# Kernel tuning notes

Measured on AMD Instinct MI355X. Metric: run time of the kernel, lower is better.

## Reference

```python
import jax, jax.numpy as jnp
import numpy as np

WEIGHT = 1.0  # config['weight']


def setup_inputs() -> dict:
    key = jax.random.key(0)
    ks = jax.random.split(key, 10)
    B, N, S, C, D, E, H, V = 8, 4096, 512, 16, 1024, 256, 1024, 100000
    return {
        "span_vecs": jax.random.normal(ks[0], (B, N, D), jnp.float32),
        "ent_table": jax.random.normal(ks[1], (V, E), jnp.float32) * 0.02,
        "W1": jax.random.normal(ks[2], (D + E, H), jnp.float32) * (1.0 / np.sqrt(D + E)),
        "b1": jnp.zeros((H,), jnp.float32),
        "W2": jax.random.normal(ks[3], (H,), jnp.float32) * (1.0 / np.sqrt(H)),
        "b2": jnp.zeros((), jnp.float32),
        "targets_all": jax.random.uniform(ks[4], (B, N, C), jnp.float32),
        "linker_indices": jax.random.randint(ks[5], (B, S), 0, N, jnp.int32),
        "candidates_all": jax.random.randint(ks[6], (B, N, C), 0, V, jnp.int32),
        "candidate_lengths_all": jax.random.randint(ks[7], (B, N), 0, C + 1, jnp.int32),
    }


def reference(span_vecs, ent_table, W1, b1, W2, b2, targets_all,
              linker_indices, candidates_all, candidate_lengths_all):
    D = span_vecs.shape[-1]
    C = candidates_all.shape[-1]
    idx = linker_indices  # [B, S]

    # batched_index_select gathers over the span axis
    candidates = jnp.take_along_axis(candidates_all, idx[:, :, None], axis=1)        # [B,S,C] int
    lengths = jnp.take_along_axis(candidate_lengths_all, idx, axis=1)                # [B,S] int
    targets = jnp.take_along_axis(targets_all, idx[:, :, None], axis=1)              # [B,S,C]
    linker_vecs = jnp.take_along_axis(span_vecs, idx[:, :, None], axis=1)            # [B,S,D]

    cand_vecs = ent_table[candidates]                                                # [B,S,C,E]

    # layers: Linear(D+E,H) -> ReLU -> (dropout=identity in eval) -> Linear(H,1)
    # fused: split W1 so the [B,S,C,D+E] expanded concat is never materialized
    W1s, W1e = W1[:D], W1[D:]
    h_span = jnp.einsum('bsd,dh->bsh', linker_vecs, W1s)                             # [B,S,H]
    h_cand = jnp.einsum('bsce,eh->bsch', cand_vecs, W1e)                             # [B,S,C,H]
    h = jax.nn.relu(h_span[:, :, None, :] + h_cand + b1)
    scores = jnp.einsum('bsch,h->bsc', h, W2) + b2                                   # [B,S,C]

    # create_candidate_mask
    mask = (jnp.arange(C)[None, None, :] < lengths[:, :, None]).astype(scores.dtype)

    # BCEWithLogitsLoss(reduction='none'), masked sum * weight
    bce = jnp.maximum(scores, 0.0) - scores * targets + jnp.log1p(jnp.exp(-jnp.abs(scores)))
    loss = (mask * bce).sum() * WEIGHT

    predictions = jnp.argmax(scores - (1.0 - mask) * 1e23, axis=-1)                  # [B,S]
    return loss, scores, predictions
```

## Files before the change

kernel.cpp:

```cpp
#include <hip/hip_runtime.h>
#include <math.h>


typedef short short8 __attribute__((ext_vector_type(8)));
typedef float f32x16 __attribute__((ext_vector_type(16)));

static __device__ inline unsigned short f2bf(float x) {
  unsigned u = __float_as_uint(x);
  unsigned r = (u + 0x7FFFu + ((u >> 16) & 1u)) >> 16;
  return (unsigned short)r;
}
static __device__ inline float bf2f(unsigned short b) {
  return __uint_as_float(((unsigned)b) << 16);
}

#define GLD_TO_LDS(gp, lp)                                          \
  __builtin_amdgcn_global_load_lds(                                 \
      (const __attribute__((address_space(1))) void*)(gp),          \
      (__attribute__((address_space(3))) void*)(lp), 16, 0, 0)

__global__ __launch_bounds__(256) void k_prep2(const int* __restrict__ linker,
                                               const int* __restrict__ cand_all,
                                               int* __restrict__ cand_ids,
                                               int* __restrict__ span_rows) {
  int g = blockIdx.x * 256 + threadIdx.x;
  int pair = g >> 4;
  int b = pair >> 9;
  int i = linker[pair];
  cand_ids[g] = cand_all[(((size_t)b << 12) + (size_t)i) * 16 + (g & 15)];
  if (g < 4096) span_rows[g] = ((g >> 9) << 12) + linker[g];
}

template <int LOG4>
__global__ __launch_bounds__(256) void k_gsplit(const float* __restrict__ src,
                                                const int* __restrict__ rows,
                                                unsigned short* __restrict__ hi,
                                                unsigned short* __restrict__ lo) {
  int f = blockIdx.x * 256 + threadIdx.x;
  int row = f >> LOG4;
  int c4 = f & ((1 << LOG4) - 1);
  const float4 v =
      *((const float4*)(src + ((size_t)rows[row] << (LOG4 + 2))) + c4);
  unsigned short h0 = f2bf(v.x), h1 = f2bf(v.y), h2 = f2bf(v.z), h3 = f2bf(v.w);
  unsigned short l0 = f2bf(v.x - bf2f(h0)), l1 = f2bf(v.y - bf2f(h1));
  unsigned short l2 = f2bf(v.z - bf2f(h2)), l3 = f2bf(v.w - bf2f(h3));
  *(ushort4*)(hi + ((size_t)f << 2)) = make_ushort4(h0, h1, h2, h3);
  *(ushort4*)(lo + ((size_t)f << 2)) = make_ushort4(l0, l1, l2, l3);
}

__global__ __launch_bounds__(256) void k_w1t(const float* __restrict__ W1,
                                             unsigned short* __restrict__ sThi,
                                             unsigned short* __restrict__ sTlo,
                                             unsigned short* __restrict__ eThi,
                                             unsigned short* __restrict__ eTlo) {
  __shared__ float t[32][33];
  int n0 = blockIdx.x * 32, k0 = blockIdx.y * 32;
  int rr = threadIdx.x >> 5, cc = threadIdx.x & 31;
#pragma unroll
  for (int i = 0; i < 4; ++i)
    t[rr + 8 * i][cc] = W1[(size_t)(k0 + rr + 8 * i) * 1024 + n0 + cc];
  __syncthreads();
#pragma unroll
  for (int i = 0; i < 4; ++i) {
    int nl = rr + 8 * i;
    float v = t[cc][nl];
    unsigned short h = f2bf(v);
    unsigned short l = f2bf(v - bf2f(h));
    int n = n0 + nl, k = k0 + cc;
    if (k0 < 1024) {
      sThi[(size_t)n * 1024 + k] = h;
      sTlo[(size_t)n * 1024 + k] = l;
    } else {
      eThi[(size_t)n * 256 + (k - 1024)] = h;
      eTlo[(size_t)n * 256 + (k - 1024)] = l;
    }
  }
}

template <int KSTEPS, int RLA, int RLB, int MODE>
__global__ __launch_bounds__(256, 2) void k_g32(
    const unsigned short* __restrict__ Ahi, const unsigned short* __restrict__ Alo,
    const unsigned short* __restrict__ Bhi, const unsigned short* __restrict__ Blo,
    const float* __restrict__ HsIn, const float* __restrict__ b1,
    const float* __restrict__ W2, float* __restrict__ Out) {
  const int tid = threadIdx.x;
  const int l = tid & 63;
  const int w = tid >> 6;
  const int wm = w >> 1, wn = w & 1;
  const int id = blockIdx.x;
  const int m8 = id & 7;
  const int cb = (id >> 3) & 7;
  const int q = id >> 6;
  const int row0 = ((q << 3) + m8) << 7;
  const int col0 = cb << 7;

  __shared__ unsigned short lds[32768];

  f32x16 acc[2][2];
#pragma unroll
  for (int i = 0; i < 2; ++i)
#pragma unroll
    for (int j = 0; j < 2; ++j)
#pragma unroll
      for (int k = 0; k < 16; ++k) acc[i][j][k] = 0.f;

  const int ar0 = tid >> 2, ap0 = tid & 3;
  const int al0c = ap0 ^ ((ar0 >> 1) & 3);
  const int ar1 = (tid + 256) >> 2;
  const int al1c = ap0 ^ ((ar1 >> 1) & 3);
  const size_t aoff0 = (size_t)(row0 + ar0) * RLA + al0c * 8;
  const size_t aoff1 = (size_t)(row0 + ar1) * RLA + al1c * 8;
  const size_t boff0 = (size_t)(col0 + ar0) * RLB + al0c * 8;
  const size_t boff1 = (size_t)(col0 + ar1) * RLB + al1c * 8;
  const int w512 = w * 512;

  {
    unsigned short* b = lds;
    GLD_TO_LDS(Ahi + aoff0, b + w512);
    GLD_TO_LDS(Ahi + aoff1, b + 2048 + w512);
    GLD_TO_LDS(Alo + aoff0, b + 4096 + w512);
    GLD_TO_LDS(Alo + aoff1, b + 6144 + w512);
    GLD_TO_LDS(Bhi + boff0, b + 8192 + w512);
    GLD_TO_LDS(Bhi + boff1, b + 10240 + w512);
    GLD_TO_LDS(Blo + boff0, b + 12288 + w512);
    GLD_TO_LDS(Blo + boff1, b + 14336 + w512);
  }
  asm volatile("s_waitcnt vmcnt(0)" ::: "memory");
  __builtin_amdgcn_s_barrier();
  asm volatile("" ::: "memory");

  for (int ks = 0; ks < KSTEPS; ++ks) {
    if (ks + 1 < KSTEPS) {
      const int k0 = (ks + 1) * 32;
      unsigned short* b = lds + (((ks + 1) & 1) << 14);
      GLD_TO_LDS(Ahi + aoff0 + k0, b + w512);
      GLD_TO_LDS(Ahi + aoff1 + k0, b + 2048 + w512);
      GLD_TO_LDS(Alo + aoff0 + k0, b + 4096 + w512);
      GLD_TO_LDS(Alo + aoff1 + k0, b + 6144 + w512);
      GLD_TO_LDS(Bhi + boff0 + k0, b + 8192 + w512);
      GLD_TO_LDS(Bhi + boff1 + k0, b + 10240 + w512);
      GLD_TO_LDS(Blo + boff0 + k0, b + 12288 + w512);
      GLD_TO_LDS(Blo + boff1 + k0, b + 14336 + w512);
    }

    const unsigned short* cbuf = lds + ((ks & 1) << 14);
#pragma unroll
    for (int kc = 0; kc < 2; ++kc) {
      const int kg = kc * 2 + (l >> 5);
      short8 ah[2], alv[2], bh[2], bl[2];
#pragma unroll
      for (int it = 0; it < 2; ++it) {
        int r = wm * 64 + it * 32 + (l & 31);
        int off = r * 32 + ((kg ^ ((r >> 1) & 3)) << 3);
        ah[it] = *(const short8*)(cbuf + off);
        alv[it] = *(const short8*)(cbuf + 4096 + off);
      }
#pragma unroll
      for (int jt = 0; jt < 2; ++jt) {
        int r = wn * 64 + jt * 32 + (l & 31);
        int off = r * 32 + ((kg ^ ((r >> 1) & 3)) << 3);
        bh[jt] = *(const short8*)(cbuf + 8192 + off);
        bl[jt] = *(const short8*)(cbuf + 12288 + off);
      }
#pragma unroll
      for (int it = 0; it < 2; ++it)
#pragma unroll
        for (int jt = 0; jt < 2; ++jt) {
          acc[it][jt] = __builtin_amdgcn_mfma_f32_32x32x16_bf16(
              ah[it], bh[jt], acc[it][jt], 0, 0, 0);
          acc[it][jt] = __builtin_amdgcn_mfma_f32_32x32x16_bf16(
              ah[it], bl[jt], acc[it][jt], 0, 0, 0);
          acc[it][jt] = __builtin_amdgcn_mfma_f32_32x32x16_bf16(
              alv[it], bh[jt], acc[it][jt], 0, 0, 0);
        }
    }

    if (ks + 1 < KSTEPS) {
      asm volatile("s_waitcnt vmcnt(0)" ::: "memory");
      __builtin_amdgcn_s_barrier();
      asm volatile("" ::: "memory");
    }
  }

  if (MODE == 0) {
#pragma unroll
    for (int it = 0; it < 2; ++it) {
      int mb = row0 + wm * 64 + it * 32 + 4 * (l >> 5);
#pragma unroll
      for (int jt = 0; jt < 2; ++jt) {
        int n = col0 + wn * 64 + jt * 32 + (l & 31);
#pragma unroll
        for (int rg = 0; rg < 16; ++rg) {
          int m = mb + (rg & 3) + 8 * (rg >> 2);
          Out[(size_t)m * 1024 + n] = acc[it][jt][rg];
        }
      }
    }
  } else {
    float sv[2][16];
#pragma unroll
    for (int it = 0; it < 2; ++it) {
#pragma unroll
      for (int rg = 0; rg < 16; ++rg) sv[it][rg] = 0.f;
      const int p0 = (row0 + wm * 64 + it * 32) >> 4;
#pragma unroll
      for (int jt = 0; jt < 2; ++jt) {
        int n = col0 + wn * 64 + jt * 32 + (l & 31);
        float b1v = b1[n], w2v = W2[n];
        float add0 = HsIn[(size_t)p0 * 1024 + n] + b1v;
        float add1 = HsIn[(size_t)(p0 + 1) * 1024 + n] + b1v;
#pragma unroll
        for (int rg = 0; rg < 16; ++rg) {
          float h = fmaxf(acc[it][jt][rg] + (rg < 8 ? add0 : add1), 0.f);
          sv[it][rg] = fmaf(h, w2v, sv[it][rg]);
        }
      }
    }
    __syncthreads();
    float* scf = (float*)lds;
    const int cc0 = l & 31, lh4 = 4 * (l >> 5);
#pragma unroll
    for (int it = 0; it < 2; ++it)
#pragma unroll
      for (int rg = 0; rg < 16; ++rg) {
        int row = (rg & 3) + 8 * (rg >> 2) + lh4;
        scf[((w * 2 + it) * 32 + row) * 32 + ((cc0 + row) & 31)] = sv[it][rg];
      }
    __syncthreads();
    int gr = tid >> 1, h = tid & 1;
    int r = gr & 31, itv = (gr >> 5) & 1, wmv = gr >> 6;
    const float* sa = scf + ((wmv * 4 + itv) * 32 + r) * 32;
    const float* sb = scf + ((wmv * 4 + 2 + itv) * 32 + r) * 32;
    float sum = 0.f;
#pragma unroll
    for (int j = 0; j < 16; ++j) {
      int cidx = (h * 16 + j + r) & 31;
      sum += sa[cidx] + sb[cidx];
    }
    sum += __shfl_xor(sum, 1, 64);
    if (h == 0) Out[(size_t)cb * 65536 + row0 + gr] = sum;
  }
}

__global__ __launch_bounds__(64) void k_final8(const float* __restrict__ score8,
                                               const float* __restrict__ b2p,
                                               const float* __restrict__ targets_all,
                                               const int* __restrict__ linker,
                                               const int* __restrict__ len_all,
                                               float* __restrict__ out) {
  int p = blockIdx.x * 64 + threadIdx.x;
  float b2 = b2p[0];
  int b = p >> 9;
  int i = linker[p];
  int len = len_all[(b << 12) + i];
  const float* tg = targets_all + ((((size_t)b << 12) + (size_t)i) << 4);

  float loss = 0.f;
  float best = -INFINITY;
  int bc = 0;
#pragma unroll
  for (int c = 0; c < 16; ++c) {
    float sc = b2;
#pragma unroll
    for (int c8 = 0; c8 < 8; ++c8) sc += score8[c8 * 65536 + p * 16 + c];
    out[1 + p * 16 + c] = sc;
    float val;
    if (c < len) {
      float t = tg[c];
      loss += fmaxf(sc, 0.f) - sc * t + log1pf(expf(-fabsf(sc)));
      val = sc;
    } else {
      val = sc - 1e23f;
    }
    if (val > best) { best = val; bc = c; }
  }
  out[1 + 65536 + p] = (float)bc;

  for (int off = 32; off > 0; off >>= 1) loss += __shfl_down(loss, off, 64);
  if (threadIdx.x == 0) atomicAdd(out, loss);
}

#define BM 128
#define BN 128
#define BK 16
#define PAD 4

__global__ __launch_bounds__(256) void k_prep(const int* __restrict__ linker,
                                              const int* __restrict__ cand_all,
                                              int* __restrict__ cand_ids) {
  int g = blockIdx.x * 256 + threadIdx.x;
  int pair = g >> 4;
  int c = g & 15;
  int b = pair >> 9;
  int i = linker[pair];
  cand_ids[g] = cand_all[(((size_t)b << 12) + (size_t)i) * 16 + c];
}

__global__ __launch_bounds__(256) void k_hs(const float* __restrict__ span,
                                            const float* __restrict__ W1,
                                            const int* __restrict__ linker,
                                            float* __restrict__ Hs) {
  const int tid = threadIdx.x;
  const int tx = tid & 15, ty = tid >> 4;
  const int row0 = blockIdx.y * BM;
  const int col0 = blockIdx.x * BN;
  __shared__ float As[BK][BM + PAD];
  __shared__ float Bs[BK][BN + PAD];
  __shared__ int rows_g[BM];
  if (tid < BM) {
    int m = row0 + tid;
    int b = m >> 9;
    rows_g[tid] = (b << 12) + linker[m];
  }
  __syncthreads();
  float acc[8][8] = {};
  for (int k0 = 0; k0 < 1024; k0 += BK) {
#pragma unroll
    for (int ll = 0; ll < 2; ++ll) {
      int f = tid + ll * 256;
      int r = f >> 2;
      int kk = (f & 3) << 2;
      const float4 v = *(const float4*)(span + (size_t)rows_g[r] * 1024 + k0 + kk);
      As[kk + 0][r] = v.x; As[kk + 1][r] = v.y;
      As[kk + 2][r] = v.z; As[kk + 3][r] = v.w;
    }
#pragma unroll
    for (int ll = 0; ll < 2; ++ll) {
      int f = tid + ll * 256;
      int kk = f >> 5;
      int nn = (f & 31) << 2;
      *(float4*)&Bs[kk][nn] = *(const float4*)(W1 + (size_t)(k0 + kk) * 1024 + col0 + nn);
    }
    __syncthreads();
#pragma unroll
    for (int k = 0; k < BK; ++k) {
      float a[8], b[8];
      *(float4*)&a[0] = *(const float4*)&As[k][ty * 8];
      *(float4*)&a[4] = *(const float4*)&As[k][ty * 8 + 4];
      *(float4*)&b[0] = *(const float4*)&Bs[k][tx * 8];
      *(float4*)&b[4] = *(const float4*)&Bs[k][tx * 8 + 4];
#pragma unroll
      for (int i = 0; i < 8; ++i)
#pragma unroll
        for (int j = 0; j < 8; ++j) acc[i][j] = fmaf(a[i], b[j], acc[i][j]);
    }
    __syncthreads();
  }
#pragma unroll
  for (int i = 0; i < 8; ++i) {
    int m = row0 + ty * 8 + i;
    float* dst = Hs + (size_t)m * 1024 + col0 + tx * 8;
    *(float4*)dst = *(float4*)&acc[i][0];
    *(float4*)(dst + 4) = *(float4*)&acc[i][4];
  }
}

__global__ __launch_bounds__(256) void k_hc(const float* __restrict__ ent,
                                            const float* __restrict__ W1,
                                            const int* __restrict__ cand_ids,
                                            const float* __restrict__ Hs,
                                            const float* __restrict__ b1,
                                            const float* __restrict__ W2,
                                            float* __restrict__ score_ws) {
  const int tid = threadIdx.x;
  const int tx = tid & 15, ty = tid >> 4;
  const int row0 = blockIdx.y * BM;
  const int col0 = blockIdx.x * BN;
  __shared__ float As[BK][BM + PAD];
  __shared__ float Bs[BK][BN + PAD];
  __shared__ int rows_g[BM];
  __shared__ float red[BM][17];
  if (tid < BM) rows_g[tid] = cand_ids[row0 + tid];
  __syncthreads();
  float acc[8][8] = {};
  for (int k0 = 0; k0 < 256; k0 += BK) {
#pragma unroll
    for (int ll = 0; ll < 2; ++ll) {
      int f = tid + ll * 256;
      int r = f >> 2;
      int kk = (f & 3) << 2;
      const float4 v = *(const float4*)(ent + (size_t)rows_g[r] * 256 + k0 + kk);
      As[kk + 0][r] = v.x; As[kk + 1][r] = v.y;
      As[kk + 2][r] = v.z; As[kk + 3][r] = v.w;
    }
#pragma unroll
    for (int ll = 0; ll < 2; ++ll) {
      int f = tid + ll * 256;
      int kk = f >> 5;
      int nn = (f & 31) << 2;
      *(float4*)&Bs[kk][nn] =
          *(const float4*)(W1 + (size_t)(1024 + k0 + kk) * 1024 + col0 + nn);
    }
    __syncthreads();
#pragma unroll
    for (int k = 0; k < BK; ++k) {
      float a[8], b[8];
      *(float4*)&a[0] = *(const float4*)&As[k][ty * 8];
      *(float4*)&a[4] = *(const float4*)&As[k][ty * 8 + 4];
      *(float4*)&b[0] = *(const float4*)&Bs[k][tx * 8];
      *(float4*)&b[4] = *(const float4*)&Bs[k][tx * 8 + 4];
#pragma unroll
      for (int i = 0; i < 8; ++i)
#pragma unroll
        for (int j = 0; j < 8; ++j) acc[i][j] = fmaf(a[i], b[j], acc[i][j]);
    }
    __syncthreads();
  }
  const int pair = (row0 + ty * 8) >> 4;
  float hsv[8], b1v[8], w2v[8];
  {
    const float* hp = Hs + (size_t)pair * 1024 + col0 + tx * 8;
    *(float4*)&hsv[0] = *(const float4*)hp;
    *(float4*)&hsv[4] = *(const float4*)(hp + 4);
    const float* bp = b1 + col0 + tx * 8;
    *(float4*)&b1v[0] = *(const float4*)bp;
    *(float4*)&b1v[4] = *(const float4*)(bp + 4);
    const float* wp = W2 + col0 + tx * 8;
    *(float4*)&w2v[0] = *(const float4*)wp;
    *(float4*)&w2v[4] = *(const float4*)(wp + 4);
  }
#pragma unroll
  for (int i = 0; i < 8; ++i) {
    float s = 0.f;
#pragma unroll
    for (int j = 0; j < 8; ++j) {
      float h = acc[i][j] + hsv[j] + b1v[j];
      h = fmaxf(h, 0.f);
      s = fmaf(h, w2v[j], s);
    }
    red[ty * 8 + i][tx] = s;
  }
  __syncthreads();
  if (tid < BM) {
    float s = 0.f;
#pragma unroll
    for (int x = 0; x < 16; ++x) s += red[tid][x];
    atomicAdd(&score_ws[row0 + tid], s);
  }
}

__global__ __launch_bounds__(256) void k_final(const float* __restrict__ score_ws,
                                               const float* __restrict__ b2p,
                                               const float* __restrict__ targets_all,
                                               const int* __restrict__ linker,
                                               const int* __restrict__ len_all,
                                               float* __restrict__ out) {
  int p = blockIdx.x * 256 + threadIdx.x;
  float b2 = b2p[0];
  int b = p >> 9;
  int i = linker[p];
  int len = len_all[(b << 12) + i];
  const float* tg = targets_all + ((((size_t)b << 12) + (size_t)i) << 4);

  float loss = 0.f;
  float best = -INFINITY;
  int bc = 0;
#pragma unroll
  for (int c = 0; c < 16; ++c) {
    float sc = score_ws[p * 16 + c] + b2;
    out[1 + p * 16 + c] = sc;
    float val;
    if (c < len) {
      float t = tg[c];
      loss += fmaxf(sc, 0.f) - sc * t + log1pf(expf(-fabsf(sc)));
      val = sc;
    } else {
      val = sc - 1e23f;
    }
    if (val > best) { best = val; bc = c; }
  }
  out[1 + 65536 + p] = (float)bc;

  for (int off = 32; off > 0; off >>= 1) loss += __shfl_down(loss, off, 64);
  if ((threadIdx.x & 63) == 0) atomicAdd(out, loss);
}

extern "C" void kernel_launch(void* const* d_in, const int* in_sizes, int n_in,
                              void* d_out, int out_size, void* d_ws,
                              size_t ws_size, hipStream_t stream) {
  const float* span    = (const float*)d_in[0];
  const float* ent     = (const float*)d_in[1];
  const float* W1      = (const float*)d_in[2];
  const float* b1      = (const float*)d_in[3];
  const float* W2      = (const float*)d_in[4];
  const float* b2      = (const float*)d_in[5];
  const float* targets = (const float*)d_in[6];
  const int* linker    = (const int*)d_in[7];
  const int* cand_all  = (const int*)d_in[8];
  const int* len_all   = (const int*)d_in[9];
  float* out = (float*)d_out;

  char* ws = (char*)d_ws;
  float* Hs       = (float*)(ws + 0);
  float* score_ws = (float*)(ws + 16777216);
  int* cand_ids   = (int*)(ws + 17039360);
  int* span_rows  = (int*)(ws + 17301504);
  unsigned short* A1h  = (unsigned short*)(ws + 17317888);
  unsigned short* A1l  = (unsigned short*)(ws + 25706496);
  unsigned short* A2h  = (unsigned short*)(ws + 34095104);
  unsigned short* A2l  = (unsigned short*)(ws + 67649536);
  unsigned short* sTh  = (unsigned short*)(ws + 101203968);
  unsigned short* sTl  = (unsigned short*)(ws + 103301120);
  unsigned short* eTh  = (unsigned short*)(ws + 105398272);
  unsigned short* eTl  = (unsigned short*)(ws + 105922560);
  const size_t NEED_MFMA = 106446848;
  float* score8 = (float*)A1h;

  hipMemsetAsync(d_out, 0, sizeof(float), stream);

  if (ws_size >= NEED_MFMA) {
    k_prep2<<<dim3(256), dim3(256), 0, stream>>>(linker, cand_all, cand_ids,
                                                 span_rows);
    k_gsplit<6><<<dim3(16384), dim3(256), 0, stream>>>(ent, cand_ids, A2h, A2l);
    k_gsplit<8><<<dim3(4096), dim3(256), 0, stream>>>(span, span_rows, A1h, A1l);
    k_w1t<<<dim3(32, 40), dim3(256), 0, stream>>>(W1, sTh, sTl, eTh, eTl);
    k_g32<32, 1024, 1024, 0><<<dim3(256), dim3(256), 0, stream>>>(
        A1h, A1l, sTh, sTl, nullptr, nullptr, nullptr, Hs);
    k_g32<8, 256, 256, 1><<<dim3(4096), dim3(256), 0, stream>>>(
        A2h, A2l, eTh, eTl, Hs, b1, W2, score8);
    k_final8<<<dim3(64), dim3(64), 0, stream>>>(score8, b2, targets, linker,
                                                len_all, out);
  } else {
    hipMemsetAsync(score_ws, 0, 65536 * sizeof(float), stream);
    k_prep<<<dim3(256), dim3(256), 0, stream>>>(linker, cand_all, cand_ids);
    dim3 g1(8, 32);
    k_hs<<<g1, dim3(256), 0, stream>>>(span, W1, linker, Hs);
    dim3 g2(8, 512);
    k_hc<<<g2, dim3(256), 0, stream>>>(ent, W1, cand_ids, Hs, b1, W2, score_ws);
    k_final<<<dim3(16), dim3(256), 0, stream>>>(score_ws, b2, targets, linker,
                                                len_all, out);
  }
}
```

Before: 401.7 us.

## Use single-pass fp16 MFMA for candidate GEMM instead of split bf16

```diff
diff --git a/kernel.cpp b/kernel.cpp
--- a/kernel.cpp
+++ b/kernel.cpp
@@ -3,6 +3,7 @@
 
 
 typedef short short8 __attribute__((ext_vector_type(8)));
+typedef _Float16 half8v __attribute__((ext_vector_type(8)));
 typedef float f32x16 __attribute__((ext_vector_type(16)));
 
 static __device__ inline unsigned short f2bf(float x) {
@@ -12,6 +13,10 @@
 }
 static __device__ inline float bf2f(unsigned short b) {
   return __uint_as_float(((unsigned)b) << 16);
+}
+static __device__ inline unsigned short f2h(float x) {
+  _Float16 h = (_Float16)x;
+  return *(unsigned short*)&h;
 }
 
 #define GLD_TO_LDS(gp, lp)                                          \
@@ -48,11 +53,23 @@
   *(ushort4*)(lo + ((size_t)f << 2)) = make_ushort4(l0, l1, l2, l3);
 }
 
+template <int LOG4>
+__global__ __launch_bounds__(256) void k_gh(const float* __restrict__ src,
+                                            const int* __restrict__ rows,
+                                            unsigned short* __restrict__ dst) {
+  int f = blockIdx.x * 256 + threadIdx.x;
+  int row = f >> LOG4;
+  int c4 = f & ((1 << LOG4) - 1);
+  const float4 v =
+      *((const float4*)(src + ((size_t)rows[row] << (LOG4 + 2))) + c4);
+  *(ushort4*)(dst + ((size_t)f << 2)) =
+      make_ushort4(f2h(v.x), f2h(v.y), f2h(v.z), f2h(v.w));
+}
+
 __global__ __launch_bounds__(256) void k_w1t(const float* __restrict__ W1,
                                              unsigned short* __restrict__ sThi,
                                              unsigned short* __restrict__ sTlo,
-                                             unsigned short* __restrict__ eThi,
-                                             unsigned short* __restrict__ eTlo) {
+                                             unsigned short* __restrict__ eT16) {
   __shared__ float t[32][33];
   int n0 = blockIdx.x * 32, k0 = blockIdx.y * 32;
   int rr = threadIdx.x >> 5, cc = threadIdx.x & 31;
@@ -64,23 +81,140 @@
   for (int i = 0; i < 4; ++i) {
     int nl = rr + 8 * i;
     float v = t[cc][nl];
-    unsigned short h = f2bf(v);
-    unsigned short l = f2bf(v - bf2f(h));
     int n = n0 + nl, k = k0 + cc;
     if (k0 < 1024) {
+      unsigned short h = f2bf(v);
+      unsigned short l = f2bf(v - bf2f(h));
       sThi[(size_t)n * 1024 + k] = h;
       sTlo[(size_t)n * 1024 + k] = l;
     } else {
-      eThi[(size_t)n * 256 + (k - 1024)] = h;
-      eTlo[(size_t)n * 256 + (k - 1024)] = l;
-    }
-  }
-}
-
-template <int KSTEPS, int RLA, int RLB, int MODE>
+      eT16[(size_t)n * 256 + (k - 1024)] = f2h(v);
+    }
+  }
+}
+
+template <int KSTEPS, int RLA, int RLB>
 __global__ __launch_bounds__(256, 2) void k_g32(
     const unsigned short* __restrict__ Ahi, const unsigned short* __restrict__ Alo,
     const unsigned short* __restrict__ Bhi, const unsigned short* __restrict__ Blo,
+    float* __restrict__ Out) {
+  const int tid = threadIdx.x;
+  const int l = tid & 63;
+  const int w = tid >> 6;
+  const int wm = w >> 1, wn = w & 1;
+  const int id = blockIdx.x;
+  const int m8 = id & 7;
+  const int cb = (id >> 3) & 7;
+  const int q = id >> 6;
+  const int row0 = ((q << 3) + m8) << 7;
+  const int col0 = cb << 7;
+
+  __shared__ unsigned short lds[32768];
+
+  f32x16 acc[2][2];
+#pragma unroll
+  for (int i = 0; i < 2; ++i)
+#pragma unroll
+    for (int j = 0; j < 2; ++j)
+#pragma unroll
+      for (int k = 0; k < 16; ++k) acc[i][j][k] = 0.f;
+
+  const int ar0 = tid >> 2, ap0 = tid & 3;
+  const int al0c = ap0 ^ ((ar0 >> 1) & 3);
+  const int ar1 = (tid + 256) >> 2;
+  const int al1c = ap0 ^ ((ar1 >> 1) & 3);
+  const size_t aoff0 = (size_t)(row0 + ar0) * RLA + al0c * 8;
+  const size_t aoff1 = (size_t)(row0 + ar1) * RLA + al1c * 8;
+  const size_t boff0 = (size_t)(col0 + ar0) * RLB + al0c * 8;
+  const size_t boff1 = (size_t)(col0 + ar1) * RLB + al1c * 8;
+  const int w512 = w * 512;
+
+  {
+    unsigned short* b = lds;
+    GLD_TO_LDS(Ahi + aoff0, b + w512);
+    GLD_TO_LDS(Ahi + aoff1, b + 2048 + w512);
+    GLD_TO_LDS(Alo + aoff0, b + 4096 + w512);
+    GLD_TO_LDS(Alo + aoff1, b + 6144 + w512);
+    GLD_TO_LDS(Bhi + boff0, b + 8192 + w512);
+    GLD_TO_LDS(Bhi + boff1, b + 10240 + w512);
+    GLD_TO_LDS(Blo + boff0, b + 12288 + w512);
+    GLD_TO_LDS(Blo + boff1, b + 14336 + w512);
+  }
+  asm volatile("s_waitcnt vmcnt(0)" ::: "memory");
+  __builtin_amdgcn_s_barrier();
+  asm volatile("" ::: "memory");
+
+  for (int ks = 0; ks < KSTEPS; ++ks) {
+    if (ks + 1 < KSTEPS) {
+      const int k0 = (ks + 1) * 32;
+      unsigned short* b = lds + (((ks + 1) & 1) << 14);
+      GLD_TO_LDS(Ahi + aoff0 + k0, b + w512);
+      GLD_TO_LDS(Ahi + aoff1 + k0, b + 2048 + w512);
+      GLD_TO_LDS(Alo + aoff0 + k0, b + 4096 + w512);
+      GLD_TO_LDS(Alo + aoff1 + k0, b + 6144 + w512);
+      GLD_TO_LDS(Bhi + boff0 + k0, b + 8192 + w512);
+      GLD_TO_LDS(Bhi + boff1 + k0, b + 10240 + w512);
+      GLD_TO_LDS(Blo + boff0 + k0, b + 12288 + w512);
+      GLD_TO_LDS(Blo + boff1 + k0, b + 14336 + w512);
+    }
+
+    const unsigned short* cbuf = lds + ((ks & 1) << 14);
+#pragma unroll
+    for (int kc = 0; kc < 2; ++kc) {
+      const int kg = kc * 2 + (l >> 5);
+      short8 ah[2], alv[2], bh[2], bl[2];
+#pragma unroll
+      for (int it = 0; it < 2; ++it) {
+        int r = wm * 64 + it * 32 + (l & 31);
+        int off = r * 32 + ((kg ^ ((r >> 1) & 3)) << 3);
+        ah[it] = *(const short8*)(cbuf + off);
+        alv[it] = *(const short8*)(cbuf + 4096 + off);
+      }
+#pragma unroll
+      for (int jt = 0; jt < 2; ++jt) {
+        int r = wn * 64 + jt * 32 + (l & 31);
+        int off = r * 32 + ((kg ^ ((r >> 1) & 3)) << 3);
+        bh[jt] = *(const short8*)(cbuf + 8192 + off);
+        bl[jt] = *(const short8*)(cbuf + 12288 + off);
+      }
+#pragma unroll
+      for (int it = 0; it < 2; ++it)
+#pragma unroll
+        for (int jt = 0; jt < 2; ++jt) {
+          acc[it][jt] = __builtin_amdgcn_mfma_f32_32x32x16_bf16(
+              ah[it], bh[jt], acc[it][jt], 0, 0, 0);
+          acc[it][jt] = __builtin_amdgcn_mfma_f32_32x32x16_bf16(
+              ah[it], bl[jt], acc[it][jt], 0, 0, 0);
+          acc[it][jt] = __builtin_amdgcn_mfma_f32_32x32x16_bf16(
+              alv[it], bh[jt], acc[it][jt], 0, 0, 0);
+        }
+    }
+
+    if (ks + 1 < KSTEPS) {
+      asm volatile("s_waitcnt vmcnt(0)" ::: "memory");
+      __builtin_amdgcn_s_barrier();
+      asm volatile("" ::: "memory");
+    }
+  }
+
+#pragma unroll
+  for (int it = 0; it < 2; ++it) {
+    int mb = row0 + wm * 64 + it * 32 + 4 * (l >> 5);
+#pragma unroll
+    for (int jt = 0; jt < 2; ++jt) {
+      int n = col0 + wn * 64 + jt * 32 + (l & 31);
+#pragma unroll
+      for (int rg = 0; rg < 16; ++rg) {
+        int m = mb + (rg & 3) + 8 * (rg >> 2);
+        Out[(size_t)m * 1024 + n] = acc[it][jt][rg];
+      }
+    }
+  }
+}
+
+__global__ __launch_bounds__(256, 4) void k_gf16(
+    const unsigned short* __restrict__ A,
+    const unsigned short* __restrict__ Bt,
     const float* __restrict__ HsIn, const float* __restrict__ b1,
     const float* __restrict__ W2, float* __restrict__ Out) {
   const int tid = threadIdx.x;
@@ -94,7 +228,7 @@
   const int row0 = ((q << 3) + m8) << 7;
   const int col0 = cb << 7;
 
-  __shared__ unsigned short lds[32768];
+  __shared__ unsigned short lds[16384];
 
   f32x16 acc[2][2];
 #pragma unroll
@@ -108,138 +242,105 @@
   const int al0c = ap0 ^ ((ar0 >> 1) & 3);
   const int ar1 = (tid + 256) >> 2;
   const int al1c = ap0 ^ ((ar1 >> 1) & 3);
-  const size_t aoff0 = (size_t)(row0 + ar0) * RLA + al0c * 8;
-  const size_t aoff1 = (size_t)(row0 + ar1) * RLA + al1c * 8;
-  const size_t boff0 = (size_t)(col0 + ar0) * RLB + al0c * 8;
-  const size_t boff1 = (size_t)(col0 + ar1) * RLB + al1c * 8;
+  const size_t aoff0 = (size_t)(row0 + ar0) * 256 + al0c * 8;
+  const size_t aoff1 = (size_t)(row0 + ar1) * 256 + al1c * 8;
+  const size_t boff0 = (size_t)(col0 + ar0) * 256 + al0c * 8;
+  const size_t boff1 = (size_t)(col0 + ar1) * 256 + al1c * 8;
   const int w512 = w * 512;
 
-  {
-    unsigned short* b = lds;
-    GLD_TO_LDS(Ahi + aoff0, b + w512);
-    GLD_TO_LDS(Ahi + aoff1, b + 2048 + w512);
-    GLD_TO_LDS(Alo + aoff0, b + 4096 + w512);
-    GLD_TO_LDS(Alo + aoff1, b + 6144 + w512);
-    GLD_TO_LDS(Bhi + boff0, b + 8192 + w512);
-    GLD_TO_LDS(Bhi + boff1, b + 10240 + w512);
-    GLD_TO_LDS(Blo + boff0, b + 12288 + w512);
-    GLD_TO_LDS(Blo + boff1, b + 14336 + w512);
-  }
+  GLD_TO_LDS(A + aoff0, lds + w512);
+  GLD_TO_LDS(A + aoff1, lds + 2048 + w512);
+  GLD_TO_LDS(Bt + boff0, lds + 4096 + w512);
+  GLD_TO_LDS(Bt + boff1, lds + 6144 + w512);
   asm volatile("s_waitcnt vmcnt(0)" ::: "memory");
   __builtin_amdgcn_s_barrier();
   asm volatile("" ::: "memory");
 
-  for (int ks = 0; ks < KSTEPS; ++ks) {
-    if (ks + 1 < KSTEPS) {
+#pragma unroll 2
+  for (int ks = 0; ks < 8; ++ks) {
+    if (ks + 1 < 8) {
       const int k0 = (ks + 1) * 32;
-      unsigned short* b = lds + (((ks + 1) & 1) << 14);
-      GLD_TO_LDS(Ahi + aoff0 + k0, b + w512);
-      GLD_TO_LDS(Ahi + aoff1 + k0, b + 2048 + w512);
-      GLD_TO_LDS(Alo + aoff0 + k0, b + 4096 + w512);
-      GLD_TO_LDS(Alo + aoff1 + k0, b + 6144 + w512);
-      GLD_TO_LDS(Bhi + boff0 + k0, b + 8192 + w512);
-      GLD_TO_LDS(Bhi + boff1 + k0, b + 10240 + w512);
-      GLD_TO_LDS(Blo + boff0 + k0, b + 12288 + w512);
-      GLD_TO_LDS(Blo + boff1 + k0, b + 14336 + w512);
-    }
-
-    const unsigned short* cbuf = lds + ((ks & 1) << 14);
+      unsigned short* b = lds + (((ks + 1) & 1) << 13);
+      GLD_TO_LDS(A + aoff0 + k0, b + w512);
+      GLD_TO_LDS(A + aoff1 + k0, b + 2048 + w512);
+      GLD_TO_LDS(Bt + boff0 + k0, b + 4096 + w512);
+      GLD_TO_LDS(Bt + boff1 + k0, b + 6144 + w512);
+    }
+
+    const unsigned short* cbuf = lds + ((ks & 1) << 13);
 #pragma unroll
     for (int kc = 0; kc < 2; ++kc) {
       const int kg = kc * 2 + (l >> 5);
-      short8 ah[2], alv[2], bh[2], bl[2];
+      half8v av[2], bv[2];
 #pragma unroll
       for (int it = 0; it < 2; ++it) {
         int r = wm * 64 + it * 32 + (l & 31);
         int off = r * 32 + ((kg ^ ((r >> 1) & 3)) << 3);
-        ah[it] = *(const short8*)(cbuf + off);
-        alv[it] = *(const short8*)(cbuf + 4096 + off);
+        av[it] = *(const half8v*)(cbuf + off);
       }
 #pragma unroll
       for (int jt = 0; jt < 2; ++jt) {
         int r = wn * 64 + jt * 32 + (l & 31);
         int off = r * 32 + ((kg ^ ((r >> 1) & 3)) << 3);
-        bh[jt] = *(const short8*)(cbuf + 8192 + off);
-        bl[jt] = *(const short8*)(cbuf + 12288 + off);
+        bv[jt] = *(const half8v*)(cbuf + 4096 + off);
       }
 #pragma unroll
       for (int it = 0; it < 2; ++it)
 #pragma unroll
-        for (int jt = 0; jt < 2; ++jt) {
-          acc[it][jt] = __builtin_amdgcn_mfma_f32_32x32x16_bf16(
-              ah[it], bh[jt], acc[it][jt], 0, 0, 0);
-          acc[it][jt] = __builtin_amdgcn_mfma_f32_32x32x16_bf16(
-              ah[it], bl[jt], acc[it][jt], 0, 0, 0);
-          acc[it][jt] = __builtin_amdgcn_mfma_f32_32x32x16_bf16(
-              alv[it], bh[jt], acc[it][jt], 0, 0, 0);
-        }
-    }
-
-    if (ks + 1 < KSTEPS) {
+        for (int jt = 0; jt < 2; ++jt)
+          acc[it][jt] = __builtin_amdgcn_mfma_f32_32x32x16_f16(
+              av[it], bv[jt], acc[it][jt], 0, 0, 0);
+    }
+
+    if (ks + 1 < 8) {
       asm volatile("s_waitcnt vmcnt(0)" ::: "memory");
       __builtin_amdgcn_s_barrier();
       asm volatile("" ::: "memory");
     }
   }
 
-  if (MODE == 0) {
-#pragma unroll
-    for (int it = 0; it < 2; ++it) {
-      int mb = row0 + wm * 64 + it * 32 + 4 * (l >> 5);
-#pragma unroll
-      for (int jt = 0; jt < 2; ++jt) {
-        int n = col0 + wn * 64 + jt * 32 + (l & 31);
-#pragma unroll
-        for (int rg = 0; rg < 16; ++rg) {
-          int m = mb + (rg & 3) + 8 * (rg >> 2);
-          Out[(size_t)m * 1024 + n] = acc[it][jt][rg];
-        }
+  float sv[2][16];
+#pragma unroll
+  for (int it = 0; it < 2; ++it) {
+#pragma unroll
+    for (int rg = 0; rg < 16; ++rg) sv[it][rg] = 0.f;
+    const int p0 = (row0 + wm * 64 + it * 32) >> 4;
+#pragma unroll
+    for (int jt = 0; jt < 2; ++jt) {
+      int n = col0 + wn * 64 + jt * 32 + (l & 31);
+      float b1v = b1[n], w2v = W2[n];
+      float add0 = HsIn[(size_t)p0 * 1024 + n] + b1v;
+      float add1 = HsIn[(size_t)(p0 + 1) * 1024 + n] + b1v;
+#pragma unroll
+      for (int rg = 0; rg < 16; ++rg) {
+        float h = fmaxf(acc[it][jt][rg] + (rg < 8 ? add0 : add1), 0.f);
+        sv[it][rg] = fmaf(h, w2v, sv[it][rg]);
       }
     }
-  } else {
-    float sv[2][16];
-#pragma unroll
-    for (int it = 0; it < 2; ++it) {
-#pragma unroll
-      for (int rg = 0; rg < 16; ++rg) sv[it][rg] = 0.f;
-      const int p0 = (row0 + wm * 64 + it * 32) >> 4;
-#pragma unroll
-      for (int jt = 0; jt < 2; ++jt) {
-        int n = col0 + wn * 64 + jt * 32 + (l & 31);
-        float b1v = b1[n], w2v = W2[n];
-        float add0 = HsIn[(size_t)p0 * 1024 + n] + b1v;
-        float add1 = HsIn[(size_t)(p0 + 1) * 1024 + n] + b1v;
-#pragma unroll
-        for (int rg = 0; rg < 16; ++rg) {
-          float h = fmaxf(acc[it][jt][rg] + (rg < 8 ? add0 : add1), 0.f);
-          sv[it][rg] = fmaf(h, w2v, sv[it][rg]);
-        }
-      }
-    }
-    __syncthreads();
-    float* scf = (float*)lds;
-    const int cc0 = l & 31, lh4 = 4 * (l >> 5);
-#pragma unroll
-    for (int it = 0; it < 2; ++it)
-#pragma unroll
-      for (int rg = 0; rg < 16; ++rg) {
-        int row = (rg & 3) + 8 * (rg >> 2) + lh4;
-        scf[((w * 2 + it) * 32 + row) * 32 + ((cc0 + row) & 31)] = sv[it][rg];
-      }
-    __syncthreads();
-    int gr = tid >> 1, h = tid & 1;
-    int r = gr & 31, itv = (gr >> 5) & 1, wmv = gr >> 6;
-    const float* sa = scf + ((wmv * 4 + itv) * 32 + r) * 32;
-    const float* sb = scf + ((wmv * 4 + 2 + itv) * 32 + r) * 32;
-    float sum = 0.f;
-#pragma unroll
-    for (int j = 0; j < 16; ++j) {
-      int cidx = (h * 16 + j + r) & 31;
-      sum += sa[cidx] + sb[cidx];
-    }
-    sum += __shfl_xor(sum, 1, 64);
-    if (h == 0) Out[(size_t)cb * 65536 + row0 + gr] = sum;
-  }
+  }
+  __syncthreads();
+  float* scf = (float*)lds;
+  const int cc0 = l & 31, lh4 = 4 * (l >> 5);
+#pragma unroll
+  for (int it = 0; it < 2; ++it)
+#pragma unroll
+    for (int rg = 0; rg < 16; ++rg) {
+      int row = (rg & 3) + 8 * (rg >> 2) + lh4;
+      scf[((w * 2 + it) * 32 + row) * 32 + ((cc0 + row) & 31)] = sv[it][rg];
+    }
+  __syncthreads();
+  int gr = tid >> 1, h = tid & 1;
+  int r = gr & 31, itv = (gr >> 5) & 1, wmv = gr >> 6;
+  const float* sa = scf + ((wmv * 4 + itv) * 32 + r) * 32;
+  const float* sb = scf + ((wmv * 4 + 2 + itv) * 32 + r) * 32;
+  float sum = 0.f;
+#pragma unroll
+  for (int j = 0; j < 16; ++j) {
+    int cidx = (h * 16 + j + r) & 31;
+    sum += sa[cidx] + sb[cidx];
+  }
+  sum += __shfl_xor(sum, 1, 64);
+  if (h == 0) Out[(size_t)cb * 65536 + row0 + gr] = sum;
 }
 
 __global__ __launch_bounds__(64) void k_final8(const float* __restrict__ score8,
@@ -497,12 +598,10 @@
   int* span_rows  = (int*)(ws + 17301504);
   unsigned short* A1h  = (unsigned short*)(ws + 17317888);
   unsigned short* A1l  = (unsigned short*)(ws + 25706496);
-  unsigned short* A2h  = (unsigned short*)(ws + 34095104);
-  unsigned short* A2l  = (unsigned short*)(ws + 67649536);
+  unsigned short* A2   = (unsigned short*)(ws + 34095104);
   unsigned short* sTh  = (unsigned short*)(ws + 101203968);
   unsigned short* sTl  = (unsigned short*)(ws + 103301120);
-  unsigned short* eTh  = (unsigned short*)(ws + 105398272);
-  unsigned short* eTl  = (unsigned short*)(ws + 105922560);
+  unsigned short* eT16 = (unsigned short*)(ws + 105398272);
   const size_t NEED_MFMA = 106446848;
   float* score8 = (float*)A1h;
 
@@ -511,13 +610,12 @@
   if (ws_size >= NEED_MFMA) {
     k_prep2<<<dim3(256), dim3(256), 0, stream>>>(linker, cand_all, cand_ids,
                                                  span_rows);
-    k_gsplit<6><<<dim3(16384), dim3(256), 0, stream>>>(ent, cand_ids, A2h, A2l);
+    k_gh<6><<<dim3(16384), dim3(256), 0, stream>>>(ent, cand_ids, A2);
     k_gsplit<8><<<dim3(4096), dim3(256), 0, stream>>>(span, span_rows, A1h, A1l);
-    k_w1t<<<dim3(32, 40), dim3(256), 0, stream>>>(W1, sTh, sTl, eTh, eTl);
-    k_g32<32, 1024, 1024, 0><<<dim3(256), dim3(256), 0, stream>>>(
-        A1h, A1l, sTh, sTl, nullptr, nullptr, nullptr, Hs);
-    k_g32<8, 256, 256, 1><<<dim3(4096), dim3(256), 0, stream>>>(
-        A2h, A2l, eTh, eTl, Hs, b1, W2, score8);
+    k_w1t<<<dim3(32, 40), dim3(256), 0, stream>>>(W1, sTh, sTl, eT16);
+    k_g32<32, 1024, 1024><<<dim3(256), dim3(256), 0, stream>>>(
+        A1h, A1l, sTh, sTl, Hs);
+    k_gf16<<<dim3(4096), dim3(256), 0, stream>>>(A2, eT16, Hs, b1, W2, score8);
     k_final8<<<dim3(64), dim3(64), 0, stream>>>(score8, b2, targets, linker,
                                                 len_all, out);
   } else {
```

New measurement: 344.7 us. -14.2%, faster.
